# Performance work log

Hardware: AMD Instinct MI355X
Metric: run time of the kernel (lower is better)

Reference implementation:

```python
import jax, jax.numpy as jnp
import numpy as np

N, K, NB, C, L, H = 10000, 32, 64, 128, 3, 64  # atoms, neighbors, basis, channels, num l-orders, MLP hidden
AVG_AGGREGATE_NUM = 10.0
LN_EPS = 1e-5
MAX_ELEM = 300


def setup_inputs() -> dict:
    key = jax.random.key(0)
    ks = jax.random.split(key, 12)
    return {
        'atomic_numbers': jax.random.randint(ks[0], (N,), 0, MAX_ELEM),
        'edge_vec': jax.random.normal(ks[1], (N, K, 3), jnp.float32),
        'f_sparse_idx_node': jax.random.randint(ks[2], (N, K), 0, N),
        'attn_mask': jax.random.randint(ks[3], (N, K, 1), 0, 2) == 1,
        'edge_scalars': jax.random.normal(ks[4], (N, K, NB), jnp.float32),
        'src_emb': jax.random.normal(ks[5], (MAX_ELEM, NB), jnp.float32),
        'tgt_emb': jax.random.normal(ks[6], (MAX_ELEM, NB), jnp.float32),
        'W1': jax.random.normal(ks[7], (L, 3 * NB, H), jnp.float32) / np.sqrt(3 * NB),
        'b1': jnp.zeros((L, H), jnp.float32),
        'g1': jnp.ones((L, H), jnp.float32),
        'be1': jnp.zeros((L, H), jnp.float32),
        'W2': jax.random.normal(ks[8], (L, H, H), jnp.float32) / np.sqrt(H),
        'b2': jnp.zeros((L, H), jnp.float32),
        'g2': jnp.ones((L, H), jnp.float32),
        'be2': jnp.zeros((L, H), jnp.float32),
        'W3': jax.random.normal(ks[9], (L, H, C), jnp.float32) / np.sqrt(H),
        'b3': jnp.zeros((L, C), jnp.float32),
    }


def _layer_norm(x, g, b):
    mu = jnp.mean(x, axis=-1, keepdims=True)
    var = jnp.var(x, axis=-1, keepdims=True)
    return (x - mu) * jax.lax.rsqrt(var + LN_EPS) * g + b


def _sph_harmonics(unit):
    """e3nn real spherical harmonics l=0,1,2, normalization='norm' (unit input vecs)."""
    x, y, z = unit[..., 0], unit[..., 1], unit[..., 2]
    s3 = float(np.sqrt(3.0))
    y0 = jnp.ones_like(x)[..., None]                       # (N,K,1)
    y1 = jnp.stack([y, z, x], axis=-1)                      # (N,K,3)
    y2 = jnp.stack([s3 * x * y,
                    s3 * y * z,
                    0.5 * (3.0 * z * z - 1.0),
                    s3 * x * z,
                    0.5 * s3 * (x * x - y * y)], axis=-1)   # (N,K,5)
    return [y0, y1, y2]


def reference(atomic_numbers, edge_vec, f_sparse_idx_node, attn_mask, edge_scalars,
              src_emb, tgt_emb, W1, b1, g1, be1, W2, b2, g2, be2, W3, b3):
    n, k = edge_scalars.shape[:2]
    # gather atom-type embeddings: target per center atom, source per neighbor
    tgt = jnp.broadcast_to(tgt_emb[atomic_numbers][:, None, :], (n, k, tgt_emb.shape[1]))
    src = src_emb[atomic_numbers][f_sparse_idx_node]            # (N,K,NB)
    edge_dis_embed = jnp.concatenate([edge_scalars, tgt, src], axis=-1)  # (N,K,3*NB)

    unit = edge_vec / jnp.linalg.norm(edge_vec, axis=-1, keepdims=True)
    sh = _sph_harmonics(unit)

    feats = []
    for i in range(W1.shape[0]):  # small fixed loop over l = 0..lmax
        h = jax.nn.silu(_layer_norm(edge_dis_embed @ W1[i] + b1[i], g1[i], be1[i]))
        h = jax.nn.silu(_layer_norm(h @ W2[i] + b2[i], g2[i], be2[i]))
        h = h @ W3[i] + b3[i]                                   # (N,K,C)
        h = jnp.where(attn_mask, 0.0, h)                        # mask padded neighbors
        feats.append(jnp.einsum('mnd,mnh->mdh', sh[i], h))      # (N,2l+1,C)
    return jnp.concatenate(feats, axis=1) / AVG_AGGREGATE_NUM   # (N,9,C)
```

## Files before the change

### kernel.cpp

```cpp
#include <hip/hip_runtime.h>
#include <hip/hip_bf16.h>


typedef __attribute__((ext_vector_type(8))) short bf16x8;
typedef __attribute__((ext_vector_type(4))) short bf16x4;
typedef __attribute__((ext_vector_type(4))) float f32x4;

__device__ __forceinline__ unsigned short f2bf(float f) {
  __hip_bfloat16 h = __float2bfloat16(f);
  return *reinterpret_cast<unsigned short*>(&h);
}

__global__ __launch_bounds__(256) void prep_weights(
    const float* __restrict__ W1, const float* __restrict__ W2,
    const float* __restrict__ W3, unsigned short* __restrict__ wf) {
  int idx = blockIdx.x * 256 + threadIdx.x;
  if (idx >= 73728) return;
  float val;
  if (idx < 36864) {
    int l = idx / 12288, r = idx % 12288;
    int blk = r >> 9, e = r & 511;
    int Nt = blk / 6, Ks = blk % 6;
    int lane = e >> 3, j = e & 7;
    int k = Ks * 32 + (lane >> 4) * 8 + j;
    int nn = Nt * 16 + (lane & 15);
    val = W1[l * 192 * 64 + k * 64 + nn];
  } else if (idx < 49152) {
    int t = idx - 36864;
    int l = t / 4096, r = t % 4096;
    int blk = r >> 9, e = r & 511;
    int Nt = blk >> 1, Ks = blk & 1;
    int lane = e >> 3, j = e & 7;
    int k = Ks * 32 + (lane >> 4) * 8 + j;
    int nn = Nt * 16 + (lane & 15);
    val = W2[l * 64 * 64 + k * 64 + nn];
  } else {
    int t = idx - 49152;
    int l = t / 8192, r = t % 8192;
    int blk = r >> 9, e = r & 511;
    int Nt = blk >> 1, Ks = blk & 1;
    int lane = e >> 3, j = e & 7;
    int k = Ks * 32 + (lane >> 4) * 8 + j;
    int nn = Nt * 16 + (lane & 15);
    val = W3[l * 64 * 128 + k * 128 + nn];
  }
  wf[idx] = f2bf(val);
}

__global__ __launch_bounds__(256) void sniff_mask(const unsigned int* __restrict__ m,
                                                  int* __restrict__ flag) {
  __shared__ int cOther, cFloat;
  if (threadIdx.x == 0) { cOther = 0; cFloat = 0; }
  __syncthreads();
  int other = 0, flt = 0;
#pragma unroll
  for (int i = 0; i < 8; ++i) {
    unsigned int w = m[threadIdx.x * 8 + i];
    if (w == 0x3F800000u) flt++;
    else if (w > 1u) other++;
  }
  if (other) atomicAdd(&cOther, other);
  if (flt)   atomicAdd(&cFloat, flt);
  __syncthreads();
  if (threadIdx.x == 0) {
    int f;
    if (cOther == 0 && cFloat == 0) f = 0;
    else if (cFloat > cOther)       f = 2;
    else                            f = 1;
    *flag = f;
  }
}

__device__ __forceinline__ bf16x8 cvt8(float4 a, float4 b) {
  bf16x8 r;
  r[0] = (short)f2bf(a.x); r[1] = (short)f2bf(a.y);
  r[2] = (short)f2bf(a.z); r[3] = (short)f2bf(a.w);
  r[4] = (short)f2bf(b.x); r[5] = (short)f2bf(b.y);
  r[6] = (short)f2bf(b.z); r[7] = (short)f2bf(b.w);
  return r;
}

__device__ __forceinline__ void ln_silu_reg(
    const f32x4* acc, const float* __restrict__ bb, const float* __restrict__ gg,
    const float* __restrict__ be, unsigned short* HbW, int e, int g) {
  float v[16]; float s = 0.f, s2 = 0.f;
#pragma unroll
  for (int mt = 0; mt < 4; ++mt) {
    float4 b4 = *reinterpret_cast<const float4*>(bb + mt * 16 + 4 * g);
    const float* b4p = reinterpret_cast<const float*>(&b4);
#pragma unroll
    for (int i = 0; i < 4; ++i) {
      float x = acc[mt][i] + b4p[i];
      v[mt * 4 + i] = x; s += x; s2 += x * x;
    }
  }
  s  += __shfl_xor(s, 16);  s2 += __shfl_xor(s2, 16);
  s  += __shfl_xor(s, 32);  s2 += __shfl_xor(s2, 32);
  float mu  = s * 0.015625f;
  float var = s2 * 0.015625f - mu * mu;
  float rstd = rsqrtf(var + 1e-5f);
#pragma unroll
  for (int mt = 0; mt < 4; ++mt) {
    float4 g4 = *reinterpret_cast<const float4*>(gg + mt * 16 + 4 * g);
    float4 e4 = *reinterpret_cast<const float4*>(be + mt * 16 + 4 * g);
    const float* g4p = reinterpret_cast<const float*>(&g4);
    const float* e4p = reinterpret_cast<const float*>(&e4);
    bf16x4 pk;
#pragma unroll
    for (int i = 0; i < 4; ++i) {
      float y  = (v[mt * 4 + i] - mu) * rstd * g4p[i] + e4p[i];
      float sl = y * (1.0f / (1.0f + __expf(-y)));
      pk[i] = (short)f2bf(sl);
    }
    *reinterpret_cast<bf16x4*>(HbW + e * 72 + mt * 16 + 4 * g) = pk;
  }
}

#define MFMA __builtin_amdgcn_mfma_f32_16x16x32_bf16

__global__ __launch_bounds__(256, 4) void edge_net_kernel(
    const int*   __restrict__ an_arr,
    const float* __restrict__ edge_vec,
    const int*   __restrict__ f_idx,
    const void*  __restrict__ attn_mask,
    const float* __restrict__ edge_scalars,
    const float* __restrict__ src_emb,
    const float* __restrict__ tgt_emb,
    const float* __restrict__ b1, const float* __restrict__ g1, const float* __restrict__ be1,
    const float* __restrict__ b2, const float* __restrict__ g2, const float* __restrict__ be2,
    const float* __restrict__ b3,
    const unsigned short* __restrict__ wf,
    const int* __restrict__ mask_flag,
    float* __restrict__ out, int Nat) {

  __shared__ __align__(16) unsigned short Hb[4][16 * 72];
  __shared__ __align__(16) unsigned short H3T[2][128 * 40];
  __shared__ __align__(16) unsigned short shT[2][16 * 40];

  const int tid  = threadIdx.x;
  const int wave = tid >> 6, lane = tid & 63;
  const int e = lane & 15, g = lane >> 4;
  const int a = wave >> 1, h = wave & 1;
  int n = blockIdx.x * 2 + a;
  const bool valid = (n < Nat);
  if (!valid) n = Nat - 1;
  const int k = h * 16 + e;

  const int an   = an_arr[n];
  const int srcA = an_arr[f_idx[n * 32 + k]];
  const int mflag = *mask_flag;
  bool masked;
  if (mflag == 0)      masked = ((const int*)attn_mask)[n * 32 + k] != 0;
  else if (mflag == 1) masked = ((const unsigned char*)attn_mask)[n * 32 + k] != 0;
  else                 masked = ((const float*)attn_mask)[n * 32 + k] != 0.0f;
  const float mf = masked ? 0.0f : 1.0f;

  {
    const float* ev = edge_vec + ((size_t)n * 32 + k) * 3;
    float ex = ev[0], ey = ev[1], ez = ev[2];
    float rn = rsqrtf(ex * ex + ey * ey + ez * ez);
    float x = ex * rn, y = ey * rn, z = ez * rn;
    const float s3 = 1.7320508075688772f;
    float s[9];
    s[0] = 1.f; s[1] = y; s[2] = z; s[3] = x;
    s[4] = s3 * x * y; s[5] = s3 * y * z; s[6] = 1.5f * z * z - 0.5f;
    s[7] = s3 * x * z; s[8] = 0.5f * s3 * (x * x - y * y);
    if (g < 3) {
#pragma unroll
      for (int q = 0; q < 3; ++q)
        shT[a][(g * 3 + q) * 40 + k] = f2bf(s[g * 3 + q] * mf);
    }
  }

  bf16x8 xf[6];
  {
    const float* es = edge_scalars + ((size_t)n * 32 + k) * 64 + g * 8;
    const float4* p0 = reinterpret_cast<const float4*>(es);
    const float4* p1 = reinterpret_cast<const float4*>(es + 32);
    xf[0] = cvt8(p0[0], p0[1]);
    xf[1] = cvt8(p1[0], p1[1]);
    const float4* t0 = reinterpret_cast<const float4*>(tgt_emb + an * 64 + g * 8);
    const float4* t1 = reinterpret_cast<const float4*>(tgt_emb + an * 64 + 32 + g * 8);
    xf[2] = cvt8(t0[0], t0[1]);
    xf[3] = cvt8(t1[0], t1[1]);
    const float4* s0 = reinterpret_cast<const float4*>(src_emb + (size_t)srcA * 64 + g * 8);
    const float4* s1 = reinterpret_cast<const float4*>(src_emb + (size_t)srcA * 64 + 32 + g * 8);
    xf[4] = cvt8(s0[0], s0[1]);
    xf[5] = cvt8(s1[0], s1[1]);
  }

  unsigned short* HbW = &Hb[wave][0];

  for (int l = 0; l < 3; ++l) {
    const unsigned short* w1a = wf + l * 12288;
    const unsigned short* w2a = wf + 36864 + l * 4096;
    const unsigned short* w3a = wf + 49152 + l * 8192;

    __syncthreads();

    f32x4 acc1[4];
#pragma unroll
    for (int mt = 0; mt < 4; ++mt) acc1[mt] = (f32x4){0.f, 0.f, 0.f, 0.f};
#pragma unroll
    for (int mt = 0; mt < 4; ++mt)
#pragma unroll
      for (int ks = 0; ks < 6; ++ks) {
        bf16x8 wfr = *reinterpret_cast<const bf16x8*>(w1a + ((mt * 6 + ks) << 9) + lane * 8);
        acc1[mt] = MFMA(wfr, xf[ks], acc1[mt], 0, 0, 0);
      }
    ln_silu_reg(acc1, b1 + l * 64, g1 + l * 64, be1 + l * 64, HbW, e, g);
    asm volatile("s_waitcnt lgkmcnt(0)" ::: "memory");
    __builtin_amdgcn_sched_barrier(0);

    bf16x8 hf[2];
#pragma unroll
    for (int ks = 0; ks < 2; ++ks)
      hf[ks] = *reinterpret_cast<const bf16x8*>(HbW + e * 72 + ks * 32 + g * 8);
    f32x4 acc2[4];
#pragma unroll
    for (int mt = 0; mt < 4; ++mt) acc2[mt] = (f32x4){0.f, 0.f, 0.f, 0.f};
#pragma unroll
    for (int mt = 0; mt < 4; ++mt)
#pragma unroll
      for (int ks = 0; ks < 2; ++ks) {
        bf16x8 wfr = *reinterpret_cast<const bf16x8*>(w2a + ((mt * 2 + ks) << 9) + lane * 8);
        acc2[mt] = MFMA(wfr, hf[ks], acc2[mt], 0, 0, 0);
      }
    ln_silu_reg(acc2, b2 + l * 64, g2 + l * 64, be2 + l * 64, HbW, e, g);
    asm volatile("s_waitcnt lgkmcnt(0)" ::: "memory");
    __builtin_amdgcn_sched_barrier(0);

#pragma unroll
    for (int ks = 0; ks < 2; ++ks)
      hf[ks] = *reinterpret_cast<const bf16x8*>(HbW + e * 72 + ks * 32 + g * 8);
    f32x4 acc3[8];
#pragma unroll
    for (int mt = 0; mt < 8; ++mt) acc3[mt] = (f32x4){0.f, 0.f, 0.f, 0.f};
#pragma unroll
    for (int mt = 0; mt < 8; ++mt)
#pragma unroll
      for (int ks = 0; ks < 2; ++ks) {
        bf16x8 wfr = *reinterpret_cast<const bf16x8*>(w3a + ((mt * 2 + ks) << 9) + lane * 8);
        acc3[mt] = MFMA(wfr, hf[ks], acc3[mt], 0, 0, 0);
      }
#pragma unroll
    for (int mt = 0; mt < 8; ++mt) {
      float4 bb = *reinterpret_cast<const float4*>(b3 + l * 128 + mt * 16 + 4 * g);
      const float* bbp = reinterpret_cast<const float*>(&bb);
#pragma unroll
      for (int i = 0; i < 4; ++i)
        H3T[a][(mt * 16 + 4 * g + i) * 40 + k] = f2bf(acc3[mt][i] + bbp[i]);
    }
    __syncthreads();

    bf16x8 af = *reinterpret_cast<const bf16x8*>(&shT[a][(lane & 15) * 40 + g * 8]);
    const int lo = l * l, hi = l * l + 2 * l;
#pragma unroll
    for (int nt = 0; nt < 4; ++nt) {
      bf16x8 bfr = *reinterpret_cast<const bf16x8*>(
          &H3T[a][(h * 64 + nt * 16 + (lane & 15)) * 40 + g * 8]);
      f32x4 ez = (f32x4){0.f, 0.f, 0.f, 0.f};
      ez = MFMA(af, bfr, ez, 0, 0, 0);
#pragma unroll
      for (int i = 0; i < 4; ++i) {
        int d = 4 * g + i;
        if (valid && d >= lo && d <= hi)
          out[((size_t)n * 9 + d) * 128 + h * 64 + nt * 16 + (lane & 15)] = 0.1f * ez[i];
      }
    }
  }
}

extern "C" void kernel_launch(void* const* d_in, const int* in_sizes, int n_in,
                              void* d_out, int out_size, void* d_ws, size_t ws_size,
                              hipStream_t stream) {
  const int*   atomic_numbers = (const int*)  d_in[0];
  const float* edge_vec       = (const float*)d_in[1];
  const int*   f_idx          = (const int*)  d_in[2];
  const void*  attn_mask      = d_in[3];
  const float* edge_scalars   = (const float*)d_in[4];
  const float* src_emb        = (const float*)d_in[5];
  const float* tgt_emb        = (const float*)d_in[6];
  const float* W1  = (const float*)d_in[7];
  const float* b1  = (const float*)d_in[8];
  const float* g1  = (const float*)d_in[9];
  const float* be1 = (const float*)d_in[10];
  const float* W2  = (const float*)d_in[11];
  const float* b2  = (const float*)d_in[12];
  const float* g2  = (const float*)d_in[13];
  const float* be2 = (const float*)d_in[14];
  const float* W3  = (const float*)d_in[15];
  const float* b3  = (const float*)d_in[16];

  unsigned short* wf = (unsigned short*)d_ws;
  int* mask_flag = ((int*)d_ws) + 36864;
  float* out = (float*)d_out;
  const int N = in_sizes[0];

  prep_weights<<<288, 256, 0, stream>>>(W1, W2, W3, wf);
  sniff_mask<<<1, 256, 0, stream>>>((const unsigned int*)attn_mask, mask_flag);
  edge_net_kernel<<<(N + 1) / 2, 256, 0, stream>>>(
      atomic_numbers, edge_vec, f_idx, attn_mask, edge_scalars,
      src_emb, tgt_emb, b1, g1, be1, b2, g2, be2, b3, wf, mask_flag, out, N);
}
```

Measured before the change: 185.3 us.

## Split l-orders across blocks and stage per-l weights in LDS

Each block now handles one l-order for 4 atoms with 512 threads, instead of looping over all 3 l-orders for 2 atoms. The block copies that l's bf16 weights (about 48KB) and its bias/LN params into shared memory, so the MFMA weight fragments come from LDS rather than global/L2. The intent is to cut repeated global weight reads and spread work over more blocks. In exchange, each atom's input gather, embedding conversion and SH computation is now done three times, and the large shared footprint limits occupancy.

```diff
diff --git a/kernel.cpp b/kernel.cpp
--- a/kernel.cpp
+++ b/kernel.cpp
@@ -81,8 +81,8 @@
 }
 
 __device__ __forceinline__ void ln_silu_reg(
-    const f32x4* acc, const float* __restrict__ bb, const float* __restrict__ gg,
-    const float* __restrict__ be, unsigned short* HbW, int e, int g) {
+    const f32x4* acc, const float* bb, const float* gg, const float* be,
+    unsigned short* HbW, int e, int g) {
   float v[16]; float s = 0.f, s2 = 0.f;
 #pragma unroll
   for (int mt = 0; mt < 4; ++mt) {
@@ -118,7 +118,7 @@
 
 #define MFMA __builtin_amdgcn_mfma_f32_16x16x32_bf16
 
-__global__ __launch_bounds__(256, 4) void edge_net_kernel(
+__global__ __launch_bounds__(512, 2) void edge_net_kernel(
     const int*   __restrict__ an_arr,
     const float* __restrict__ edge_vec,
     const int*   __restrict__ f_idx,
@@ -133,18 +133,48 @@
     const int* __restrict__ mask_flag,
     float* __restrict__ out, int Nat) {
 
-  __shared__ __align__(16) unsigned short Hb[4][16 * 72];
-  __shared__ __align__(16) unsigned short H3T[2][128 * 40];
-  __shared__ __align__(16) unsigned short shT[2][16 * 40];
+  __shared__ __align__(16) unsigned short WL[24576];
+  __shared__ __align__(16) float BL[512];
+  __shared__ __align__(16) unsigned short Hb[8][16 * 72];
+  __shared__ __align__(16) unsigned short H3T[4][128 * 40];
+  __shared__ __align__(16) unsigned short shT[4][16 * 40];
 
   const int tid  = threadIdx.x;
   const int wave = tid >> 6, lane = tid & 63;
   const int e = lane & 15, g = lane >> 4;
   const int a = wave >> 1, h = wave & 1;
-  int n = blockIdx.x * 2 + a;
+  const int chunk = blockIdx.x / 3;
+  const int l = blockIdx.x - chunk * 3;
+  int n = chunk * 4 + a;
   const bool valid = (n < Nat);
   if (!valid) n = Nat - 1;
   const int k = h * 16 + e;
+
+  {
+    const uint4* s1 = reinterpret_cast<const uint4*>(wf + l * 12288);
+    const uint4* s2 = reinterpret_cast<const uint4*>(wf + 36864 + l * 4096);
+    const uint4* s3 = reinterpret_cast<const uint4*>(wf + 49152 + l * 8192);
+    uint4* dst = reinterpret_cast<uint4*>(WL);
+#pragma unroll
+    for (int it = 0; it < 6; ++it) {
+      int i = it * 512 + tid;
+      uint4 v;
+      if (i < 1536)      v = s1[i];
+      else if (i < 2048) v = s2[i - 1536];
+      else               v = s3[i - 2048];
+      dst[i] = v;
+    }
+    float bv;
+    int t = tid >> 6, o = tid & 63;
+    if (tid < 384) {
+      const float* p = (t == 0) ? b1 : (t == 1) ? g1 : (t == 2) ? be1
+                     : (t == 3) ? b2 : (t == 4) ? g2 : be2;
+      bv = p[l * 64 + o];
+    } else {
+      bv = b3[l * 128 + (tid - 384)];
+    }
+    BL[tid] = bv;
+  }
 
   const int an   = an_arr[n];
   const int srcA = an_arr[f_idx[n * 32 + k]];
@@ -160,11 +190,11 @@
     float ex = ev[0], ey = ev[1], ez = ev[2];
     float rn = rsqrtf(ex * ex + ey * ey + ez * ez);
     float x = ex * rn, y = ey * rn, z = ez * rn;
-    const float s3 = 1.7320508075688772f;
+    const float s3c = 1.7320508075688772f;
     float s[9];
     s[0] = 1.f; s[1] = y; s[2] = z; s[3] = x;
-    s[4] = s3 * x * y; s[5] = s3 * y * z; s[6] = 1.5f * z * z - 0.5f;
-    s[7] = s3 * x * z; s[8] = 0.5f * s3 * (x * x - y * y);
+    s[4] = s3c * x * y; s[5] = s3c * y * z; s[6] = 1.5f * z * z - 0.5f;
+    s[7] = s3c * x * z; s[8] = 0.5f * s3c * (x * x - y * y);
     if (g < 3) {
 #pragma unroll
       for (int q = 0; q < 3; ++q)
@@ -189,84 +219,84 @@
     xf[5] = cvt8(s1[0], s1[1]);
   }
 
+  __syncthreads();
+
   unsigned short* HbW = &Hb[wave][0];
-
-  for (int l = 0; l < 3; ++l) {
-    const unsigned short* w1a = wf + l * 12288;
-    const unsigned short* w2a = wf + 36864 + l * 4096;
-    const unsigned short* w3a = wf + 49152 + l * 8192;
-
-    __syncthreads();
-
-    f32x4 acc1[4];
-#pragma unroll
-    for (int mt = 0; mt < 4; ++mt) acc1[mt] = (f32x4){0.f, 0.f, 0.f, 0.f};
-#pragma unroll
-    for (int mt = 0; mt < 4; ++mt)
-#pragma unroll
-      for (int ks = 0; ks < 6; ++ks) {
-        bf16x8 wfr = *reinterpret_cast<const bf16x8*>(w1a + ((mt * 6 + ks) << 9) + lane * 8);
-        acc1[mt] = MFMA(wfr, xf[ks], acc1[mt], 0, 0, 0);
-      }
-    ln_silu_reg(acc1, b1 + l * 64, g1 + l * 64, be1 + l * 64, HbW, e, g);
-    asm volatile("s_waitcnt lgkmcnt(0)" ::: "memory");
-    __builtin_amdgcn_sched_barrier(0);
-
-    bf16x8 hf[2];
-#pragma unroll
-    for (int ks = 0; ks < 2; ++ks)
-      hf[ks] = *reinterpret_cast<const bf16x8*>(HbW + e * 72 + ks * 32 + g * 8);
-    f32x4 acc2[4];
-#pragma unroll
-    for (int mt = 0; mt < 4; ++mt) acc2[mt] = (f32x4){0.f, 0.f, 0.f, 0.f};
-#pragma unroll
-    for (int mt = 0; mt < 4; ++mt)
-#pragma unroll
-      for (int ks = 0; ks < 2; ++ks) {
-        bf16x8 wfr = *reinterpret_cast<const bf16x8*>(w2a + ((mt * 2 + ks) << 9) + lane * 8);
-        acc2[mt] = MFMA(wfr, hf[ks], acc2[mt], 0, 0, 0);
-      }
-    ln_silu_reg(acc2, b2 + l * 64, g2 + l * 64, be2 + l * 64, HbW, e, g);
-    asm volatile("s_waitcnt lgkmcnt(0)" ::: "memory");
-    __builtin_amdgcn_sched_barrier(0);
-
-#pragma unroll
-    for (int ks = 0; ks < 2; ++ks)
-      hf[ks] = *reinterpret_cast<const bf16x8*>(HbW + e * 72 + ks * 32 + g * 8);
-    f32x4 acc3[8];
-#pragma unroll
-    for (int mt = 0; mt < 8; ++mt) acc3[mt] = (f32x4){0.f, 0.f, 0.f, 0.f};
-#pragma unroll
-    for (int mt = 0; mt < 8; ++mt)
-#pragma unroll
-      for (int ks = 0; ks < 2; ++ks) {
-        bf16x8 wfr = *reinterpret_cast<const bf16x8*>(w3a + ((mt * 2 + ks) << 9) + lane * 8);
-        acc3[mt] = MFMA(wfr, hf[ks], acc3[mt], 0, 0, 0);
-      }
-#pragma unroll
-    for (int mt = 0; mt < 8; ++mt) {
-      float4 bb = *reinterpret_cast<const float4*>(b3 + l * 128 + mt * 16 + 4 * g);
-      const float* bbp = reinterpret_cast<const float*>(&bb);
-#pragma unroll
-      for (int i = 0; i < 4; ++i)
-        H3T[a][(mt * 16 + 4 * g + i) * 40 + k] = f2bf(acc3[mt][i] + bbp[i]);
-    }
-    __syncthreads();
-
-    bf16x8 af = *reinterpret_cast<const bf16x8*>(&shT[a][(lane & 15) * 40 + g * 8]);
-    const int lo = l * l, hi = l * l + 2 * l;
-#pragma unroll
-    for (int nt = 0; nt < 4; ++nt) {
-      bf16x8 bfr = *reinterpret_cast<const bf16x8*>(
-          &H3T[a][(h * 64 + nt * 16 + (lane & 15)) * 40 + g * 8]);
-      f32x4 ez = (f32x4){0.f, 0.f, 0.f, 0.f};
-      ez = MFMA(af, bfr, ez, 0, 0, 0);
-#pragma unroll
-      for (int i = 0; i < 4; ++i) {
-        int d = 4 * g + i;
-        if (valid && d >= lo && d <= hi)
-          out[((size_t)n * 9 + d) * 128 + h * 64 + nt * 16 + (lane & 15)] = 0.1f * ez[i];
-      }
+  const unsigned short* w1a = WL;
+  const unsigned short* w2a = WL + 12288;
+  const unsigned short* w3a = WL + 16384;
+  const float* b1l = BL;        const float* g1l = BL + 64;  const float* be1l = BL + 128;
+  const float* b2l = BL + 192;  const float* g2l = BL + 256; const float* be2l = BL + 320;
+  const float* b3l = BL + 384;
+
+  f32x4 acc1[4];
+#pragma unroll
+  for (int mt = 0; mt < 4; ++mt) acc1[mt] = (f32x4){0.f, 0.f, 0.f, 0.f};
+#pragma unroll
+  for (int mt = 0; mt < 4; ++mt)
+#pragma unroll
+    for (int ks = 0; ks < 6; ++ks) {
+      bf16x8 wfr = *reinterpret_cast<const bf16x8*>(w1a + ((mt * 6 + ks) << 9) + lane * 8);
+      acc1[mt] = MFMA(wfr, xf[ks], acc1[mt], 0, 0, 0);
+    }
+  ln_silu_reg(acc1, b1l, g1l, be1l, HbW, e, g);
+  asm volatile("s_waitcnt lgkmcnt(0)" ::: "memory");
+  __builtin_amdgcn_sched_barrier(0);
+
+  bf16x8 hf[2];
+#pragma unroll
+  for (int ks = 0; ks < 2; ++ks)
+    hf[ks] = *reinterpret_cast<const bf16x8*>(HbW + e * 72 + ks * 32 + g * 8);
+  f32x4 acc2[4];
+#pragma unroll
+  for (int mt = 0; mt < 4; ++mt) acc2[mt] = (f32x4){0.f, 0.f, 0.f, 0.f};
+#pragma unroll
+  for (int mt = 0; mt < 4; ++mt)
+#pragma unroll
+    for (int ks = 0; ks < 2; ++ks) {
+      bf16x8 wfr = *reinterpret_cast<const bf16x8*>(w2a + ((mt * 2 + ks) << 9) + lane * 8);
+      acc2[mt] = MFMA(wfr, hf[ks], acc2[mt], 0, 0, 0);
+    }
+  ln_silu_reg(acc2, b2l, g2l, be2l, HbW, e, g);
+  asm volatile("s_waitcnt lgkmcnt(0)" ::: "memory");
+  __builtin_amdgcn_sched_barrier(0);
+
+#pragma unroll
+  for (int ks = 0; ks < 2; ++ks)
+    hf[ks] = *reinterpret_cast<const bf16x8*>(HbW + e * 72 + ks * 32 + g * 8);
+  f32x4 acc3[8];
+#pragma unroll
+  for (int mt = 0; mt < 8; ++mt) acc3[mt] = (f32x4){0.f, 0.f, 0.f, 0.f};
+#pragma unroll
+  for (int mt = 0; mt < 8; ++mt)
+#pragma unroll
+    for (int ks = 0; ks < 2; ++ks) {
+      bf16x8 wfr = *reinterpret_cast<const bf16x8*>(w3a + ((mt * 2 + ks) << 9) + lane * 8);
+      acc3[mt] = MFMA(wfr, hf[ks], acc3[mt], 0, 0, 0);
+    }
+#pragma unroll
+  for (int mt = 0; mt < 8; ++mt) {
+    float4 bb = *reinterpret_cast<const float4*>(b3l + mt * 16 + 4 * g);
+    const float* bbp = reinterpret_cast<const float*>(&bb);
+#pragma unroll
+    for (int i = 0; i < 4; ++i)
+      H3T[a][(mt * 16 + 4 * g + i) * 40 + k] = f2bf(acc3[mt][i] + bbp[i]);
+  }
+  __syncthreads();
+
+  bf16x8 af = *reinterpret_cast<const bf16x8*>(&shT[a][(lane & 15) * 40 + g * 8]);
+  const int lo = l * l, hi = l * l + 2 * l;
+#pragma unroll
+  for (int nt = 0; nt < 4; ++nt) {
+    bf16x8 bfr = *reinterpret_cast<const bf16x8*>(
+        &H3T[a][(h * 64 + nt * 16 + (lane & 15)) * 40 + g * 8]);
+    f32x4 ez = (f32x4){0.f, 0.f, 0.f, 0.f};
+    ez = MFMA(af, bfr, ez, 0, 0, 0);
+#pragma unroll
+    for (int i = 0; i < 4; ++i) {
+      int d = 4 * g + i;
+      if (valid && d >= lo && d <= hi)
+        out[((size_t)n * 9 + d) * 128 + h * 64 + nt * 16 + (lane & 15)] = 0.1f * ez[i];
     }
   }
 }
@@ -299,7 +329,8 @@
 
   prep_weights<<<288, 256, 0, stream>>>(W1, W2, W3, wf);
   sniff_mask<<<1, 256, 0, stream>>>((const unsigned int*)attn_mask, mask_flag);
-  edge_net_kernel<<<(N + 1) / 2, 256, 0, stream>>>(
+  const int nblocks = ((N + 3) / 4) * 3;
+  edge_net_kernel<<<nblocks, 512, 0, stream>>>(
       atomic_numbers, edge_vec, f_idx, attn_mask, edge_scalars,
       src_emb, tgt_emb, b1, g1, be1, b2, g2, be2, b3, wf, mask_flag, out, N);
 }
```

New measurement: 260.7 us. +40.7%, slower.
